# Kernel optimization log

Hardware: AMD Instinct MI355X
Metric: run time of the kernel (lower is better)

The kernel has to match this reference:

```python
import jax, jax.numpy as jnp
import numpy as np

T, D, K = 16384, 512, 128
NODES = [512, 512]


def _rnn_layer(X, Wx, Wh, bh, h0):
    # X: [T, M1] -> [T, M2]; precompute input projection (parallel part)
    Xp = X @ Wx  # [T, M2]
    def step(h, x):
        h = jax.nn.relu(x + h @ Wh + bh)
        return h, h
    _, out = jax.lax.scan(step, h0[0], Xp)
    return out  # [T, M2]


def setup_inputs() -> dict:
    key = jax.random.key(0)
    ks = jax.random.split(key, 16)
    inp = {"X": jax.random.normal(ks[0], (T, D), dtype=jnp.float32)}
    M1 = D
    for i, M2 in enumerate(NODES):
        s = 1.0 / np.sqrt(M1 + M2)
        inp[f"Wx{i}"] = jax.random.normal(ks[1 + 3 * i], (M1, M2), dtype=jnp.float32) * s
        inp[f"Wh{i}"] = jax.random.normal(ks[2 + 3 * i], (M2, M2), dtype=jnp.float32) * s
        inp[f"bh{i}"] = jnp.zeros((M2,), dtype=jnp.float32)
        inp[f"h0{i}"] = jnp.zeros((1, M2), dtype=jnp.float32)
        M1 = M2
    # nn.Linear(M1, K): weight [K, M1], bias [K]
    lim = 1.0 / np.sqrt(M1)
    inp["W_log"] = jax.random.uniform(ks[10], (K, M1), minval=-lim, maxval=lim, dtype=jnp.float32)
    inp["b_log"] = jax.random.uniform(ks[11], (K,), minval=-lim, maxval=lim, dtype=jnp.float32)
    return inp


def reference(X, Wx0, Wh0, bh0, h00, Wx1, Wh1, bh1, h01, W_log, b_log):
    h = _rnn_layer(X, Wx0, Wh0, bh0, h00)
    h = _rnn_layer(h, Wx1, Wh1, bh1, h01)
    return h @ W_log.T + b_log  # [T, K]
```

## Files before the change

### kernel.cpp

```cpp
#include <hip/hip_runtime.h>
#include <stdint.h>

#define TT 16384
#define DH 512
#define KK 128
#define SENT 0xAAAAAAAAu
#define CROWS 32
#define NCHUNK (TT / CROWS)
#define NPROJ 112
#define RSLOT 16

__device__ uint32_t g_ring[2][RSLOT][DH];
__device__ uint32_t g_flagXp[2][NCHUNK];
__device__ uint32_t g_H1u[(size_t)TT * DH];
__device__ float    g_Xp1[(size_t)TT * DH];

static __device__ __forceinline__ uint32_t aload(const uint32_t* p) {
    return __hip_atomic_load(p, __ATOMIC_RELAXED, __HIP_MEMORY_SCOPE_AGENT);
}
static __device__ __forceinline__ void astore(uint32_t* p, uint32_t v) {
    __hip_atomic_store(p, v, __ATOMIC_RELAXED, __HIP_MEMORY_SCOPE_AGENT);
}

__global__ void init_kernel() {
    const int tid = threadIdx.x + blockIdx.x * 1024;
    uint32_t* r = &g_ring[0][0][0];
    if (tid < 2 * RSLOT * DH) r[tid] = SENT;
    if (tid < 2 * NCHUNK) (&g_flagXp[0][0])[tid] = 0u;
}

union __align__(16) SMem {
    struct { float inT[DH * 36]; float wt[32 * 516]; } proj;
    struct { float h[2][8][68]; } scan;
};

static __device__ void proj_chunk(SMem& sm, const float* __restrict__ W,
                                  const float* __restrict__ src, int srcMode,
                                  float* __restrict__ dst, uint32_t* flag, int t0)
{
    const int tid = threadIdx.x;
    #pragma unroll
    for (int i = 0; i < 32; ++i) {
        int idx = tid + 512 * i;
        int row = idx >> 9;
        int col = idx & 511;
        float v;
        if (srcMode == 0) {
            v = src[(size_t)t0 * DH + idx];
        } else {
            const uint32_t* p = (const uint32_t*)src + (size_t)t0 * DH + idx;
            uint32_t u;
            while ((u = aload(p)) == SENT) __builtin_amdgcn_s_sleep(1);
            v = __uint_as_float(u);
        }
        sm.proj.inT[col * 36 + row] = v;
    }
    __syncthreads();

    const int rg = tid >> 7;
    const int cg = tid & 127;
    float acc[8][4];
    #pragma unroll
    for (int i = 0; i < 8; ++i)
        #pragma unroll
        for (int j = 0; j < 4; ++j) acc[i][j] = 0.f;

    for (int kt = 0; kt < 16; ++kt) {
        const int k0 = kt * 32;
        #pragma unroll
        for (int i = 0; i < 8; ++i) {
            int f4 = tid + 512 * i;
            int wr = f4 >> 7;
            int wc = (f4 & 127) << 2;
            *(float4*)&sm.proj.wt[wr * 516 + wc] =
                *(const float4*)&W[(size_t)(k0 + wr) * DH + wc];
        }
        __syncthreads();
        #pragma unroll 4
        for (int kk = 0; kk < 32; ++kk) {
            float4 a0 = *(const float4*)&sm.proj.inT[(k0 + kk) * 36 + (rg << 3)];
            float4 a1 = *(const float4*)&sm.proj.inT[(k0 + kk) * 36 + (rg << 3) + 4];
            float4 w  = *(const float4*)&sm.proj.wt[kk * 516 + (cg << 2)];
            float av[8] = {a0.x, a0.y, a0.z, a0.w, a1.x, a1.y, a1.z, a1.w};
            float wv[4] = {w.x, w.y, w.z, w.w};
            #pragma unroll
            for (int i = 0; i < 8; ++i)
                #pragma unroll
                for (int j = 0; j < 4; ++j) acc[i][j] += av[i] * wv[j];
        }
        __syncthreads();
    }
    #pragma unroll
    for (int i = 0; i < 8; ++i)
        #pragma unroll
        for (int j = 0; j < 4; ++j)
            astore((uint32_t*)&dst[(size_t)(t0 + (rg << 3) + i) * DH + (cg << 2) + j],
                   __float_as_uint(acc[i][j]));
    __threadfence();
    __syncthreads();
    if (tid == 0)
        __hip_atomic_store(flag, 1u, __ATOMIC_RELEASE, __HIP_MEMORY_SCOPE_AGENT);
}

__global__ __launch_bounds__(512, 1)
void fused(const float* __restrict__ X,
           const float* __restrict__ Wx0, const float* __restrict__ Wh0,
           const float* __restrict__ bh0, const float* __restrict__ h00,
           const float* __restrict__ Wx1, const float* __restrict__ Wh1,
           const float* __restrict__ bh1, const float* __restrict__ h01,
           float* H0r, float* Xp0)
{
    __shared__ SMem sm;
    const int bIdx = blockIdx.x;
    const int tid = threadIdx.x;

    if (bIdx < 16) {
        const int L    = bIdx & 1;
        const int b    = bIdx >> 1;
        const int w    = tid >> 6;
        const int lane = tid & 63;
        const int seg  = lane >> 3;
        const int m    = lane & 7;
        const int col  = (b << 6) + (w << 3) + m;
        const int pc   = (w < b) ? w : w + 1;

        const float* Wh  = L ? Wh1 : Wh0;
        const float* bhv = L ? bh1 : bh0;
        const float* h0v = L ? h01 : h00;
        uint32_t* HfulU  = L ? g_H1u : (uint32_t*)H0r;
        const float* Xp  = L ? g_Xp1 : Xp0;
        uint32_t* flagXp = g_flagXp[L];
        uint32_t (*ring)[DH] = g_ring[L];

        float wh[64];
        #pragma unroll
        for (int j = 0; j < 64; ++j)
            wh[j] = Wh[(size_t)((seg << 6) + j) * DH + col];
        const float bias = bhv[col];

        float v = h0v[col];
        float xp_cur = 0.f;
        int curCh = 0;
        if (seg == 0) {
            while (__hip_atomic_load(&flagXp[0], __ATOMIC_ACQUIRE,
                                     __HIP_MEMORY_SCOPE_AGENT) != 1u) {}
            xp_cur = Xp[col];
        }

        for (int t = 0; t < TT; ++t) {
            const int pb = t & 1;
            if (seg == 0) sm.scan.h[pb][b][(w << 3) + m] = v;
            if (w < 7) {
                float hv;
                if (t == 0) {
                    hv = h0v[(pc << 6) + lane];
                } else {
                    const uint32_t par = (uint32_t)((t - 1) >> 4) & 1u;
                    const uint32_t* p = &ring[(t - 1) & 15][(pc << 6) + lane];
                    uint32_t u;
                    do { u = aload(p); } while ((u >> 31) != par);
                    hv = __uint_as_float(u & 0x7fffffffu);
                }
                sm.scan.h[pb][pc][lane] = hv;
            }
            __syncthreads();

            float acc = 0.f;
            const float4* h4 = (const float4*)&sm.scan.h[pb][seg][0];
            #pragma unroll
            for (int r = 0; r < 16; ++r) {
                float4 hv = h4[r];
                acc += wh[4*r+0]*hv.x + wh[4*r+1]*hv.y
                     + wh[4*r+2]*hv.z + wh[4*r+3]*hv.w;
            }
            if (seg == 0) acc += bias + xp_cur;
            acc += __shfl_xor(acc, 8, 64);
            acc += __shfl_xor(acc, 16, 64);
            acc += __shfl_xor(acc, 32, 64);
            v = fmaxf(acc, 0.f);

            if (seg == 0) {
                const uint32_t hb = __float_as_uint(v);
                astore(&ring[t & 15][col],
                       hb | (((uint32_t)(t >> 4) & 1u) << 31));
                astore(HfulU + (size_t)t * DH + col, hb);
                if (t + 1 < TT) {
                    const int ch = (t + 1) >> 5;
                    if (ch != curCh) {
                        while (__hip_atomic_load(&flagXp[ch], __ATOMIC_ACQUIRE,
                                                 __HIP_MEMORY_SCOPE_AGENT) != 1u) {}
                        curCh = ch;
                    }
                    xp_cur = __uint_as_float(
                        aload((const uint32_t*)&Xp[(size_t)(t + 1) * DH + col]));
                }
            }
        }
    } else {
        const int pi = bIdx - 16;
        for (int cc = pi; cc < NCHUNK; cc += NPROJ) {
            proj_chunk(sm, Wx0, X,   0, Xp0,   &g_flagXp[0][cc], cc * CROWS);
            proj_chunk(sm, Wx1, H0r, 1, g_Xp1, &g_flagXp[1][cc], cc * CROWS);
        }
    }
}

__global__ __launch_bounds__(128, 1)
void logits_kernel(const float* __restrict__ Wl, const float* __restrict__ bl,
                   float* __restrict__ out)
{
    const float* H1 = (const float*)g_H1u;
    const int t0 = blockIdx.x * 8;
    const int k = threadIdx.x;

    __shared__ __align__(16) float hs[8 * DH];
    for (int idx = k; idx < 8 * DH / 4; idx += 128)
        ((float4*)hs)[idx] = ((const float4*)&H1[(size_t)t0 * DH])[idx];
    __syncthreads();

    float acc[8];
    const float bk = bl[k];
    #pragma unroll
    for (int r = 0; r < 8; ++r) acc[r] = bk;

    const float4* w4 = (const float4*)&Wl[(size_t)k * DH];
    for (int j = 0; j < DH / 4; ++j) {
        float4 w = w4[j];
        #pragma unroll
        for (int r = 0; r < 8; ++r) {
            float4 h = ((const float4*)&hs[r * DH])[j];
            acc[r] += w.x * h.x + w.y * h.y + w.z * h.z + w.w * h.w;
        }
    }
    #pragma unroll
    for (int r = 0; r < 8; ++r) out[(size_t)(t0 + r) * KK + k] = acc[r];
}

extern "C" void kernel_launch(void* const* d_in, const int* in_sizes, int n_in,
                              void* d_out, int out_size, void* d_ws, size_t ws_size,
                              hipStream_t stream)
{
    const float* X   = (const float*)d_in[0];
    const float* Wx0 = (const float*)d_in[1];
    const float* Wh0 = (const float*)d_in[2];
    const float* bh0 = (const float*)d_in[3];
    const float* h00 = (const float*)d_in[4];
    const float* Wx1 = (const float*)d_in[5];
    const float* Wh1 = (const float*)d_in[6];
    const float* bh1 = (const float*)d_in[7];
    const float* h01 = (const float*)d_in[8];
    const float* Wl  = (const float*)d_in[9];
    const float* bl  = (const float*)d_in[10];
    float* out = (float*)d_out;

    float* H0r = (float*)d_ws;
    float* Xp0 = H0r + (size_t)TT * DH;

    hipMemsetAsync(d_ws, 0xAA, (size_t)TT * DH * sizeof(float), stream);
    hipLaunchKernelGGL(init_kernel, dim3(17), dim3(1024), 0, stream);
    hipLaunchKernelGGL(fused, dim3(16 + NPROJ), dim3(512), 0, stream,
                       X, Wx0, Wh0, bh0, h00, Wx1, Wh1, bh1, h01, H0r, Xp0);
    hipLaunchKernelGGL(logits_kernel, dim3(TT / 8), dim3(128), 0, stream,
                       Wl, bl, out);
}
```

Measured before the change: 22.42 ms.

## Split recurrent scan across four blocks per layer with 128-column slices

Each RNN layer's sequential scan now runs on 4 blocks of 128 columns instead of 8 blocks of 64. Each thread holds 128 recurrent weights and sums over 4 segments instead of 8. The intent is to cut cross-block ring polling and the volume of the per-step exchange, since each block now gathers 384 remote values per step. The input-projection value is also prefetched two steps ahead so its load latency leaves the critical path. The cost is more register pressure per thread, more FMAs per step on the serial path, and fewer blocks sharing the scan work.

```diff
diff --git a/kernel.cpp b/kernel.cpp
--- a/kernel.cpp
+++ b/kernel.cpp
@@ -21,6 +21,9 @@
 static __device__ __forceinline__ void astore(uint32_t* p, uint32_t v) {
     __hip_atomic_store(p, v, __ATOMIC_RELAXED, __HIP_MEMORY_SCOPE_AGENT);
 }
+static __device__ __forceinline__ float aloadf(const float* p) {
+    return __uint_as_float(aload((const uint32_t*)p));
+}
 
 __global__ void init_kernel() {
     const int tid = threadIdx.x + blockIdx.x * 1024;
@@ -31,7 +34,7 @@
 
 union __align__(16) SMem {
     struct { float inT[DH * 36]; float wt[32 * 516]; } proj;
-    struct { float h[2][8][68]; } scan;
+    struct { float h[2][4 * 132]; } scan;
 };
 
 static __device__ void proj_chunk(SMem& sm, const float* __restrict__ W,
@@ -114,15 +117,14 @@
     const int bIdx = blockIdx.x;
     const int tid = threadIdx.x;
 
-    if (bIdx < 16) {
+    if (bIdx < 8) {
         const int L    = bIdx & 1;
-        const int b    = bIdx >> 1;
+        const int q    = bIdx >> 1;
         const int w    = tid >> 6;
         const int lane = tid & 63;
-        const int seg  = lane >> 3;
-        const int m    = lane & 7;
-        const int col  = (b << 6) + (w << 3) + m;
-        const int pc   = (w < b) ? w : w + 1;
+        const int seg  = lane >> 4;
+        const int m    = lane & 15;
+        const int col  = (q << 7) + (w << 4) + m;
 
         const float* Wh  = L ? Wh1 : Wh0;
         const float* bhv = L ? bh1 : bh0;
@@ -132,72 +134,76 @@
         uint32_t* flagXp = g_flagXp[L];
         uint32_t (*ring)[DH] = g_ring[L];
 
-        float wh[64];
-        #pragma unroll
-        for (int j = 0; j < 64; ++j)
-            wh[j] = Wh[(size_t)((seg << 6) + j) * DH + col];
+        const int rIdx = w * 48 + lane;
+        const int rc   = (rIdx < (q << 7)) ? rIdx : rIdx + 128;
+        const int selfCol = (q << 7) + (w << 4) + lane;
+
+        float wh[128];
+        #pragma unroll
+        for (int j = 0; j < 128; ++j)
+            wh[j] = Wh[(size_t)((seg << 7) + j) * DH + col];
         const float bias = bhv[col];
 
-        float v = h0v[col];
-        float xp_cur = 0.f;
-        int curCh = 0;
-        if (seg == 0) {
-            while (__hip_atomic_load(&flagXp[0], __ATOMIC_ACQUIRE,
-                                     __HIP_MEMORY_SCOPE_AGENT) != 1u) {}
-            xp_cur = Xp[col];
-        }
+        float v_prev = h0v[col];
+
+        while (__hip_atomic_load(&flagXp[0], __ATOMIC_ACQUIRE,
+                                 __HIP_MEMORY_SCOPE_AGENT) != 1u)
+            __builtin_amdgcn_s_sleep(1);
+        float xpA = aloadf(&Xp[col]);
+        float xpB = aloadf(&Xp[(size_t)DH + col]);
 
         for (int t = 0; t < TT; ++t) {
             const int pb = t & 1;
-            if (seg == 0) sm.scan.h[pb][b][(w << 3) + m] = v;
-            if (w < 7) {
+            float* hstage = sm.scan.h[pb];
+            if (lane < 16)
+                hstage[(selfCol >> 7) * 132 + (selfCol & 127)] = v_prev;
+            if (lane < 48) {
                 float hv;
                 if (t == 0) {
-                    hv = h0v[(pc << 6) + lane];
+                    hv = h0v[rc];
                 } else {
                     const uint32_t par = (uint32_t)((t - 1) >> 4) & 1u;
-                    const uint32_t* p = &ring[(t - 1) & 15][(pc << 6) + lane];
+                    const uint32_t* p = &ring[(t - 1) & 15][rc];
                     uint32_t u;
                     do { u = aload(p); } while ((u >> 31) != par);
                     hv = __uint_as_float(u & 0x7fffffffu);
                 }
-                sm.scan.h[pb][pc][lane] = hv;
+                hstage[(rc >> 7) * 132 + (rc & 127)] = hv;
             }
             __syncthreads();
 
             float acc = 0.f;
-            const float4* h4 = (const float4*)&sm.scan.h[pb][seg][0];
+            const float4* h4 = (const float4*)&hstage[seg * 132];
             #pragma unroll
-            for (int r = 0; r < 16; ++r) {
+            for (int r = 0; r < 32; ++r) {
                 float4 hv = h4[r];
                 acc += wh[4*r+0]*hv.x + wh[4*r+1]*hv.y
                      + wh[4*r+2]*hv.z + wh[4*r+3]*hv.w;
             }
-            if (seg == 0) acc += bias + xp_cur;
-            acc += __shfl_xor(acc, 8, 64);
             acc += __shfl_xor(acc, 16, 64);
             acc += __shfl_xor(acc, 32, 64);
-            v = fmaxf(acc, 0.f);
-
-            if (seg == 0) {
+            float v = fmaxf(acc + bias + xpA, 0.f);
+
+            if (lane < 16) {
                 const uint32_t hb = __float_as_uint(v);
                 astore(&ring[t & 15][col],
                        hb | (((uint32_t)(t >> 4) & 1u) << 31));
                 astore(HfulU + (size_t)t * DH + col, hb);
-                if (t + 1 < TT) {
-                    const int ch = (t + 1) >> 5;
-                    if (ch != curCh) {
-                        while (__hip_atomic_load(&flagXp[ch], __ATOMIC_ACQUIRE,
-                                                 __HIP_MEMORY_SCOPE_AGENT) != 1u) {}
-                        curCh = ch;
-                    }
-                    xp_cur = __uint_as_float(
-                        aload((const uint32_t*)&Xp[(size_t)(t + 1) * DH + col]));
+            }
+            v_prev = v;
+
+            xpA = xpB;
+            if (t + 2 < TT) {
+                if (((t + 2) & 31) == 0) {
+                    const uint32_t* f = &flagXp[(t + 2) >> 5];
+                    while (__hip_atomic_load(f, __ATOMIC_ACQUIRE,
+                                             __HIP_MEMORY_SCOPE_AGENT) != 1u) {}
                 }
+                xpB = aloadf(&Xp[(size_t)(t + 2) * DH + col]);
             }
         }
     } else {
-        const int pi = bIdx - 16;
+        const int pi = bIdx - 8;
         for (int cc = pi; cc < NCHUNK; cc += NPROJ) {
             proj_chunk(sm, Wx0, X,   0, Xp0,   &g_flagXp[0][cc], cc * CROWS);
             proj_chunk(sm, Wx1, H0r, 1, g_Xp1, &g_flagXp[1][cc], cc * CROWS);
@@ -258,7 +264,7 @@
 
     hipMemsetAsync(d_ws, 0xAA, (size_t)TT * DH * sizeof(float), stream);
     hipLaunchKernelGGL(init_kernel, dim3(17), dim3(1024), 0, stream);
-    hipLaunchKernelGGL(fused, dim3(16 + NPROJ), dim3(512), 0, stream,
+    hipLaunchKernelGGL(fused, dim3(8 + NPROJ), dim3(512), 0, stream,
                        X, Wx0, Wh0, bh0, h00, Wx1, Wh1, bh1, h01, H0r, Xp0);
     hipLaunchKernelGGL(logits_kernel, dim3(TT / 8), dim3(128), 0, stream,
                        Wl, bl, out);
```

Measured after the change: 28.93 ms. 1.29x slower.
